# Kernel tuning notes

Measured on AMD Instinct MI355X. Metric: run time of the kernel, lower is better.

Reference implementation:

```python
import jax, jax.numpy as jnp
import numpy as np

B, T, H = 128, 256, 512


def setup_inputs() -> dict:
    key = jax.random.key(0)
    ks = jax.random.split(key, 9)
    s = 0.05  # small init scale to keep tanh/softmax well-conditioned
    return {
        "enc_output": jax.random.normal(ks[0], (B, T, H), jnp.float32),
        "h0": jax.random.normal(ks[1], (B, H), jnp.float32) * s,
        "c0": jax.random.normal(ks[2], (B, H), jnp.float32) * s,
        "W1": jax.random.normal(ks[3], (H, H), jnp.float32) * s,
        "W2": jax.random.normal(ks[4], (H, H), jnp.float32) * s,
        "V": jax.random.normal(ks[5], (H,), jnp.float32) * s,
        "Wk": jax.random.normal(ks[6], (T, 4 * H), jnp.float32) * s,  # LSTM input kernel (input = last_pointer, dim T)
        "Wr": jax.random.normal(ks[7], (H, 4 * H), jnp.float32) * s,  # LSTM recurrent kernel
        "b": jnp.zeros((4 * H,), jnp.float32),
    }


def reference(enc_output, h0, c0, W1, W2, V, Wk, Wr, b):
    Bq, Tq, Hq = enc_output.shape
    # Precompute W1 @ encoder outputs (constant across decode steps; same math)
    w1_e = jnp.einsum("bth,hd->btd", enc_output, W1)  # [B,T,H]

    def step(carry, _):
        h, c, lp = carry  # h,c: [B,H]; lp (last pointer probs): [B,T]
        z = lp @ Wk + h @ Wr + b  # [B,4H], keras gate order i,f,g,o
        i, f, g, o = jnp.split(z, 4, axis=-1)
        c_new = jax.nn.sigmoid(f) * c + jax.nn.sigmoid(i) * jnp.tanh(g)
        h_new = jax.nn.sigmoid(o) * jnp.tanh(c_new)
        # Bahdanau additive attention -> pointer distribution over T
        w2_d = h_new @ W2  # [B,H]
        score = jnp.einsum("bth,h->bt", jnp.tanh(w1_e + w2_d[:, None, :]), V)  # [B,T]
        probs = jax.nn.softmax(score, axis=1)
        return (h_new, c_new, probs), probs

    lp0 = jnp.ones((Bq, Tq), enc_output.dtype)
    _, outs = jax.lax.scan(step, (h0, c0, lp0), None, length=Tq)  # [T,B,T]
    return jnp.transpose(outs, (1, 0, 2))  # [B, T(steps), T(pointers)]
```

## Files before the change

kernel.cpp:

```cpp
#include <hip/hip_runtime.h>
#include <hip/hip_bf16.h>
#include <cstddef>

#define B_ 128
#define T_ 256
#define H_ 512
#define H4_ 2048

__device__ __forceinline__ float rcp_f(float x) { return __builtin_amdgcn_rcpf(x); }
__device__ __forceinline__ float sigf(float x) { return rcp_f(1.0f + __expf(-x)); }
__device__ __forceinline__ float tanh_f(float x) {
  float p = __expf(x + x);
  return fmaf(-2.0f, rcp_f(1.0f + p), 1.0f);
}
__device__ __forceinline__ float4 ld4(const float* p) { return *reinterpret_cast<const float4*>(p); }
__device__ __forceinline__ void st4(float* p, float4 v) { *reinterpret_cast<float4*>(p) = v; }
__device__ __forceinline__ void fma4(float4& a, float s, float4 w) {
  a.x = fmaf(s, w.x, a.x); a.y = fmaf(s, w.y, a.y);
  a.z = fmaf(s, w.z, a.z); a.w = fmaf(s, w.w, a.w);
}

__device__ __forceinline__ float ald1(const float* p) {
  return __hip_atomic_load(p, __ATOMIC_RELAXED, __HIP_MEMORY_SCOPE_AGENT);
}
__device__ __forceinline__ void ast1(float* p, float v) {
  __hip_atomic_store(p, v, __ATOMIC_RELAXED, __HIP_MEMORY_SCOPE_AGENT);
}
__device__ __forceinline__ float2 ald2(const float* p) {
  unsigned long long v = __hip_atomic_load((const unsigned long long*)p,
                                           __ATOMIC_RELAXED, __HIP_MEMORY_SCOPE_AGENT);
  union { unsigned long long u; float2 f; } c; c.u = v; return c.f;
}

union H4 { ushort4 u; _Float16 h[4]; };
union H8 { int4 v; _Float16 h[8]; };
__device__ __forceinline__ void sth4(_Float16* p, float4 v) {
  H4 c;
  c.h[0] = (_Float16)v.x; c.h[1] = (_Float16)v.y;
  c.h[2] = (_Float16)v.z; c.h[3] = (_Float16)v.w;
  *reinterpret_cast<ushort4*>(p) = c.u;
}

#define W1EH_OFF  0ull
#define WPACK_OFF 8388608ull
#define W2H_OFF   9961472ull
#define HP_OFF    10092544ull
#define HROW_OFF  10223616ull
#define EP_OFF    10289152ull
#define D2_OFF    10321920ull
#define CNT_OFF   10322432ull

__global__ __launch_bounds__(256) void w1e_kernel(const float* __restrict__ A,
                                                  const float* __restrict__ Bw,
                                                  _Float16* __restrict__ C) {
  __shared__ float As[32][68];
  __shared__ float Bs[32][68];
  const int i0 = blockIdx.x * 64;
  const int j0 = blockIdx.y * 64;
  const int tx = threadIdx.x & 15, ty = threadIdx.x >> 4;
  float4 acc0 = make_float4(0,0,0,0), acc1 = acc0, acc2 = acc0, acc3 = acc0;
  for (int k0 = 0; k0 < H_; k0 += 32) {
#pragma unroll
    for (int q = 0; q < 2; q++) {
      int idx = q * 256 + threadIdx.x;
      int ai = idx >> 3, ak = (idx & 7) << 2;
      float4 av = ld4(A + (size_t)(i0 + ai) * H_ + k0 + ak);
      As[ak][ai] = av.x; As[ak + 1][ai] = av.y; As[ak + 2][ai] = av.z; As[ak + 3][ai] = av.w;
      int bk = idx >> 4, bj = (idx & 15) << 2;
      st4(&Bs[bk][bj], ld4(Bw + (size_t)(k0 + bk) * H_ + j0 + bj));
    }
    __syncthreads();
#pragma unroll
    for (int kk = 0; kk < 32; kk++) {
      float4 a = ld4(&As[kk][ty << 2]);
      float4 bv = ld4(&Bs[kk][tx << 2]);
      fma4(acc0, a.x, bv); fma4(acc1, a.y, bv); fma4(acc2, a.z, bv); fma4(acc3, a.w, bv);
    }
    __syncthreads();
  }
  size_t base = (size_t)(i0 + (ty << 2)) * H_ + j0 + (tx << 2);
  sth4(&C[base], acc0); sth4(&C[base + H_], acc1);
  sth4(&C[base + 2 * H_], acc2); sth4(&C[base + 3 * H_], acc3);
}

__global__ __launch_bounds__(256) void pack_kernel(const float* __restrict__ Wk,
                                                   const float* __restrict__ Wr,
                                                   const float* __restrict__ W2,
                                                   float* __restrict__ Wpack,
                                                   _Float16* __restrict__ W2h,
                                                   unsigned* __restrict__ cnt) {
  const int g = blockIdx.x, tid = threadIdx.x;
#pragma unroll
  for (int it = 0; it < 24; ++it) {
    int idx = it * 256 + tid;
    int k = idx >> 3, c = idx & 7;
    int col = (c >> 1) * 512 + 2 * g + (c & 1);
    float v = (k < 256) ? Wk[(size_t)k * H4_ + col] : Wr[(size_t)(k - 256) * H4_ + col];
    Wpack[((size_t)g * 768 + k) * 8 + c] = v;
  }
#pragma unroll
  for (int it = 0; it < 4; ++it) {
    int idx = it * 65536 + g * 256 + tid;
    W2h[idx] = (_Float16)W2[idx];
  }
  if (g == 0) {
#pragma unroll
    for (int i = 0; i < 4; ++i) cnt[i * 256 + tid] = 0u;
  }
}

__device__ __forceinline__ void gridbar(unsigned* cnt, unsigned& phase, int tid, int wg) {
  asm volatile("s_waitcnt vmcnt(0)" ::: "memory");
  __syncthreads();
  if (tid == 0) {
    unsigned r1 = __hip_atomic_fetch_add(&cnt[(wg & 31) * 16], 1u,
                                         __ATOMIC_RELAXED, __HIP_MEMORY_SCOPE_AGENT);
    if (r1 == phase * 8u + 7u) {
      unsigned r2 = __hip_atomic_fetch_add(&cnt[512], 1u,
                                           __ATOMIC_RELAXED, __HIP_MEMORY_SCOPE_AGENT);
      if (r2 == phase * 32u + 31u) {
#pragma unroll
        for (int i = 0; i < 8; ++i)
          __hip_atomic_store(&cnt[768 + i * 16], phase + 1u,
                             __ATOMIC_RELAXED, __HIP_MEMORY_SCOPE_AGENT);
      }
    }
    const unsigned* rel = &cnt[768 + (wg >> 5) * 16];
    while (__hip_atomic_load(rel, __ATOMIC_RELAXED, __HIP_MEMORY_SCOPE_AGENT) <= phase)
      __builtin_amdgcn_s_sleep(2);
  }
  __syncthreads();
  ++phase;
}

__global__ __launch_bounds__(1024, 4) void decoder_persistent(
    const _Float16* __restrict__ w1eh, const float* __restrict__ Wpack,
    const _Float16* __restrict__ W2h, const float* __restrict__ Vv,
    const float* __restrict__ bias, const float* __restrict__ h0,
    const float* __restrict__ c0,
    float* __restrict__ htr,
    float* __restrict__ hrow,
    float* __restrict__ etr,
    float* __restrict__ d2,
    unsigned* __restrict__ cnt,
    float* __restrict__ out) {
  __shared__ float smem[21504];
  float* zred     = smem;
  float* zfin     = smem + 12288;
  float* c_lds    = smem + 13312;
  float* bias_lds = smem + 13568;
  float* dred     = smem + 13576;
  float* hrow_lds = smem + 13592;
  float* w2d_lds  = smem + 14104;

  const int g = blockIdx.x;
  const int tid = threadIdx.x;
  const int bl = tid & 127;
  const int ksu = __builtin_amdgcn_readfirstlane(tid >> 7);
  const int wv = tid >> 6, ln = tid & 63;
  const int sb = g >> 1;
  const int t0 = (g & 1) << 7;
  unsigned phase = 0;
  float epv[8];

  if (tid < 256) {
    int b = tid >> 1, jj = tid & 1;
    c_lds[b * 2 + jj] = c0[(size_t)b * H_ + 2 * g + jj];
    ast1(htr + 65536 + ((size_t)g * 128 + b) * 2 + jj, h0[(size_t)b * H_ + 2 * g + jj]);
    if (g == 0) ast1(d2 + 256 + tid, 0.5f);
  }
  if (tid < 8) bias_lds[tid] = bias[(tid >> 1) * 512 + 2 * g + (tid & 1)];
  if (g < 128 && tid < 256) ast1(etr + g * 256 + tid, 1.0f);
  gridbar(cnt, phase, tid, g);

  const float4 v0 = ld4(Vv + (ln << 3));
  const float4 v1 = ld4(Vv + (ln << 3) + 4);
  const _Float16* rowb = w1eh + (((size_t)sb * 256 + t0 + (wv << 3)) << 9) + (ln << 3);

  for (int s = 0; s < 256; ++s) {
    const float* hin = htr + ((s + 1) & 1) * 65536;
    float* hout = htr + (s & 1) * 65536;
    const float* dPrev = d2 + ((s + 1) & 1) * 256;
    float* dCur = d2 + (s & 1) * 256;

    H8 raws[8];
#pragma unroll
    for (int r = 0; r < 8; ++r)
      raws[r].v = *reinterpret_cast<const int4*>(rowb + ((size_t)r << 9));

    {
      float2 dd = ald2(dPrev + bl * 2);
      float rd = rcp_f(dd.x + dd.y);
      float4 accA = make_float4(0,0,0,0), accB = accA;
      float2 e0[8], e1[8];
#pragma unroll
      for (int j = 0; j < 8; ++j) {
        int k2 = ksu * 2 + j * 16;
        e0[j] = ald2(etr + k2 * 256 + bl * 2);
        e1[j] = ald2(etr + k2 * 256 + 256 + bl * 2);
      }
#pragma unroll
      for (int j = 0; j < 8; ++j) {
        int kb = ksu * 4 + j * 32;
        const float* wp = Wpack + (((size_t)g * 768 + kb) << 3);
        float4 wa0 = ld4(wp),      wb0 = ld4(wp + 4);
        float4 wa1 = ld4(wp + 8),  wb1 = ld4(wp + 12);
        float4 wa2 = ld4(wp + 16), wb2 = ld4(wp + 20);
        float4 wa3 = ld4(wp + 24), wb3 = ld4(wp + 28);
        fma4(accA, e0[j].x, wa0); fma4(accB, e0[j].x, wb0);
        fma4(accA, e0[j].y, wa1); fma4(accB, e0[j].y, wb1);
        fma4(accA, e1[j].x, wa2); fma4(accB, e1[j].x, wb2);
        fma4(accA, e1[j].y, wa3); fma4(accB, e1[j].y, wb3);
      }
      accA.x *= rd; accA.y *= rd; accA.z *= rd; accA.w *= rd;
      accB.x *= rd; accB.y *= rd; accB.z *= rd; accB.w *= rd;
#pragma unroll
      for (int half = 0; half < 2; ++half) {
        float2 p0[8], p1[8];
#pragma unroll
        for (int j = 0; j < 8; ++j) {
          int k2 = ksu * 2 + (half * 8 + j) * 16;
          p0[j] = ald2(hin + k2 * 256 + bl * 2);
          p1[j] = ald2(hin + k2 * 256 + 256 + bl * 2);
        }
#pragma unroll
        for (int j = 0; j < 8; ++j) {
          int kb = ksu * 4 + (half * 8 + j) * 32;
          const float* wp = Wpack + (((size_t)g * 768 + 256 + kb) << 3);
          float4 wa0 = ld4(wp),      wb0 = ld4(wp + 4);
          float4 wa1 = ld4(wp + 8),  wb1 = ld4(wp + 12);
          float4 wa2 = ld4(wp + 16), wb2 = ld4(wp + 20);
          float4 wa3 = ld4(wp + 24), wb3 = ld4(wp + 28);
          fma4(accA, p0[j].x, wa0); fma4(accB, p0[j].x, wb0);
          fma4(accA, p0[j].y, wa1); fma4(accB, p0[j].y, wb1);
          fma4(accA, p1[j].x, wa2); fma4(accB, p1[j].x, wb2);
          fma4(accA, p1[j].y, wa3); fma4(accB, p1[j].y, wb3);
        }
      }
      float* zr = &zred[(ksu * 128 + bl) * 12];
      st4(zr, accA); st4(zr + 4, accB);
    }
    __syncthreads();
    {
      int b = tid >> 3, cc = tid & 7;
      float zsum = bias_lds[cc];
#pragma unroll
      for (int k2 = 0; k2 < 8; ++k2) zsum += zred[(k2 * 128 + b) * 12 + cc];
      zfin[b * 8 + cc] = zsum;
    }
    __syncthreads();
    if (tid < 256) {
      int b = tid >> 1, jj = tid & 1;
      float zi = zfin[b * 8 + 0 + jj], zf = zfin[b * 8 + 2 + jj];
      float zg = zfin[b * 8 + 4 + jj], zo = zfin[b * 8 + 6 + jj];
      float cv = c_lds[b * 2 + jj];
      float cn = sigf(zf) * cv + sigf(zi) * tanh_f(zg);
      float hn = sigf(zo) * tanh_f(cn);
      c_lds[b * 2 + jj] = cn;
      ast1(hout + ((size_t)g * 128 + b) * 2 + jj, hn);
      ast1(hrow + (size_t)b * 512 + 2 * g + jj, hn);
    }
    gridbar(cnt, phase, tid, g);

    if (tid < 256) {
      float2 hv = ald2(hrow + (size_t)sb * 512 + (tid << 1));
      hrow_lds[(tid << 1)] = hv.x; hrow_lds[(tid << 1) + 1] = hv.y;
    }
    __syncthreads();
    {
      const int c8 = ln << 3;
      const _Float16* wp = W2h + ((size_t)(wv << 5) << 9) + c8;
      const float* hb = hrow_lds + (wv << 5);
      float4 accL = make_float4(0,0,0,0), accH = accL;
#pragma unroll 4
      for (int k = 0; k < 32; ++k) {
        float hk = hb[k];
        H8 w; w.v = *reinterpret_cast<const int4*>(wp + ((size_t)k << 9));
        accL.x = fmaf(hk, (float)w.h[0], accL.x);
        accL.y = fmaf(hk, (float)w.h[1], accL.y);
        accL.z = fmaf(hk, (float)w.h[2], accL.z);
        accL.w = fmaf(hk, (float)w.h[3], accL.w);
        accH.x = fmaf(hk, (float)w.h[4], accH.x);
        accH.y = fmaf(hk, (float)w.h[5], accH.y);
        accH.z = fmaf(hk, (float)w.h[6], accH.z);
        accH.w = fmaf(hk, (float)w.h[7], accH.w);
      }
      st4(&zred[(wv << 9) + c8], accL);
      st4(&zred[(wv << 9) + c8 + 4], accH);
    }
    __syncthreads();
    if (tid < 512) {
      float s16 = 0.0f;
#pragma unroll
      for (int q = 0; q < 16; ++q) s16 += zred[(q << 9) + tid];
      w2d_lds[tid] = s16;
    }
    __syncthreads();
    {
      float4 u0 = ld4(w2d_lds + (ln << 3));
      float4 u1 = ld4(w2d_lds + (ln << 3) + 4);
      float2 ddp = ald2(dPrev + sb * 2);
      float rdp = rcp_f(ddp.x + ddp.y);
      float sc[8];
#pragma unroll
      for (int r = 0; r < 8; ++r) {
        float a;
        a = tanh_f((float)raws[r].h[0] + u0.x) * v0.x;
        a = fmaf(tanh_f((float)raws[r].h[1] + u0.y), v0.y, a);
        a = fmaf(tanh_f((float)raws[r].h[2] + u0.z), v0.z, a);
        a = fmaf(tanh_f((float)raws[r].h[3] + u0.w), v0.w, a);
        a = fmaf(tanh_f((float)raws[r].h[4] + u1.x), v1.x, a);
        a = fmaf(tanh_f((float)raws[r].h[5] + u1.y), v1.y, a);
        a = fmaf(tanh_f((float)raws[r].h[6] + u1.z), v1.z, a);
        a = fmaf(tanh_f((float)raws[r].h[7] + u1.w), v1.w, a);
#pragma unroll
        for (int m = 32; m > 0; m >>= 1) a += __shfl_xor(a, m, 64);
        sc[r] = a;
      }
      if (ln == 0) {
        float dacc = 0.0f;
#pragma unroll
        for (int r = 0; r < 8; ++r) {
          int t = t0 + (wv << 3) + r;
          if (s > 0) out[(size_t)sb * 65536 + (size_t)(s - 1) * 256 + t] = epv[r] * rdp;
          float ev = __expf(sc[r]);
          epv[r] = ev;
          ast1(etr + (((t >> 1) << 7) + sb) * 2 + (t & 1), ev);
          dacc += ev;
        }
        dred[wv] = dacc;
      }
    }
    __syncthreads();
    if (tid == 0) {
      float sd = 0.0f;
#pragma unroll
      for (int k = 0; k < 16; ++k) sd += dred[k];
      ast1(dCur + sb * 2 + (g & 1), sd);
    }
    gridbar(cnt, phase, tid, g);
  }

  {
    float2 ddf = ald2(d2 + 256 + sb * 2);
    float rdf = rcp_f(ddf.x + ddf.y);
    if (ln == 0) {
#pragma unroll
      for (int r = 0; r < 8; ++r) {
        int t = t0 + (wv << 3) + r;
        out[(size_t)sb * 65536 + 255ull * 256 + t] = epv[r] * rdf;
      }
    }
  }
}

extern "C" void kernel_launch(void* const* d_in, const int* in_sizes, int n_in,
                              void* d_out, int out_size, void* d_ws, size_t ws_size,
                              hipStream_t stream) {
  const float* enc  = (const float*)d_in[0];
  const float* h0   = (const float*)d_in[1];
  const float* c0   = (const float*)d_in[2];
  const float* W1   = (const float*)d_in[3];
  const float* W2   = (const float*)d_in[4];
  const float* V    = (const float*)d_in[5];
  const float* Wk   = (const float*)d_in[6];
  const float* Wr   = (const float*)d_in[7];
  const float* bias = (const float*)d_in[8];
  float* out = (float*)d_out;
  float* ws = (float*)d_ws;

  _Float16* w1eh = (_Float16*)(ws + W1EH_OFF);
  float* Wpack   = ws + WPACK_OFF;
  _Float16* W2h  = (_Float16*)(ws + W2H_OFF);
  float* htr     = ws + HP_OFF;
  float* hrow    = ws + HROW_OFF;
  float* etr     = ws + EP_OFF;
  float* d2      = ws + D2_OFF;
  unsigned* cnt  = (unsigned*)(ws + CNT_OFF);

  pack_kernel<<<256, 256, 0, stream>>>(Wk, Wr, W2, Wpack, W2h, cnt);
  w1e_kernel<<<dim3(512, 8), 256, 0, stream>>>(enc, W1, w1eh);
  decoder_persistent<<<256, 1024, 0, stream>>>(w1eh, Wpack, W2h, V, bias, h0, c0,
                                               htr, hrow, etr, d2, cnt, out);
}
```

Before: 10.32 ms.

## Retile LSTM gate GEMV into batch×column blocks with LDS-staged inputs

The per-step LSTM gate GEMV is repartitioned. Each workgroup now owns 16 batch rows by 16 hidden columns (64 gate columns) rather than all 128 batch rows by 2 hidden columns. The e and h inputs for those 16 rows are staged into LDS once per step, with h stored as fp16, and the repacked weight slice is reused across the rows. This removes the transposed h/e copies and the duplicate hrow store, cutting global atomic loads per step. The cost is more weight traffic per workgroup, since each now reads 64 columns × 768 rows, and an fp16 rounding of h in the gate GEMV.

```diff
diff --git a/kernel.cpp b/kernel.cpp
--- a/kernel.cpp
+++ b/kernel.cpp
@@ -32,10 +32,10 @@
   union { unsigned long long u; float2 f; } c; c.u = v; return c.f;
 }
 
-union H4 { ushort4 u; _Float16 h[4]; };
-union H8 { int4 v; _Float16 h[8]; };
+union H4u { ushort4 u; _Float16 h[4]; };
+union H8u { int4 v; _Float16 h[8]; };
 __device__ __forceinline__ void sth4(_Float16* p, float4 v) {
-  H4 c;
+  H4u c;
   c.h[0] = (_Float16)v.x; c.h[1] = (_Float16)v.y;
   c.h[2] = (_Float16)v.z; c.h[3] = (_Float16)v.w;
   *reinterpret_cast<ushort4*>(p) = c.u;
@@ -44,11 +44,10 @@
 #define W1EH_OFF  0ull
 #define WPACK_OFF 8388608ull
 #define W2H_OFF   9961472ull
-#define HP_OFF    10092544ull
-#define HROW_OFF  10223616ull
-#define EP_OFF    10289152ull
-#define D2_OFF    10321920ull
-#define CNT_OFF   10322432ull
+#define HROW_OFF  10092544ull
+#define EROW_OFF  10223616ull
+#define D2_OFF    10256384ull
+#define CNT_OFF   10256896ull
 
 __global__ __launch_bounds__(256) void w1e_kernel(const float* __restrict__ A,
                                                   const float* __restrict__ Bw,
@@ -90,13 +89,15 @@
                                                    _Float16* __restrict__ W2h,
                                                    unsigned* __restrict__ cnt) {
   const int g = blockIdx.x, tid = threadIdx.x;
+  const int gblk = g >> 3, slice = g & 7;
 #pragma unroll
   for (int it = 0; it < 24; ++it) {
     int idx = it * 256 + tid;
-    int k = idx >> 3, c = idx & 7;
-    int col = (c >> 1) * 512 + 2 * g + (c & 1);
+    int kk = idx >> 6, c = idx & 63;
+    int k = slice * 96 + kk;
+    int col = (c & 3) * 512 + gblk * 16 + (c >> 2);
     float v = (k < 256) ? Wk[(size_t)k * H4_ + col] : Wr[(size_t)(k - 256) * H4_ + col];
-    Wpack[((size_t)g * 768 + k) * 8 + c] = v;
+    Wpack[((size_t)gblk * 768 + k) * 64 + c] = v;
   }
 #pragma unroll
   for (int it = 0; it < 4; ++it) {
@@ -138,132 +139,142 @@
     const _Float16* __restrict__ W2h, const float* __restrict__ Vv,
     const float* __restrict__ bias, const float* __restrict__ h0,
     const float* __restrict__ c0,
-    float* __restrict__ htr,
-    float* __restrict__ hrow,
-    float* __restrict__ etr,
+    float* __restrict__ hrowB,
+    float* __restrict__ erow,
     float* __restrict__ d2,
     unsigned* __restrict__ cnt,
     float* __restrict__ out) {
   __shared__ float smem[21504];
-  float* zred     = smem;
-  float* zfin     = smem + 12288;
-  float* c_lds    = smem + 13312;
-  float* bias_lds = smem + 13568;
-  float* dred     = smem + 13576;
-  float* hrow_lds = smem + 13592;
-  float* w2d_lds  = smem + 14104;
+  float* zred    = smem;
+  float* zfin    = smem + 8448;
+  float* stage_e = smem + 9536;
+  _Float16* stageh = (_Float16*)(smem + 13696);
+  float* c_lds   = smem + 17856;
+  float* bias64  = smem + 18112;
+  float* d_lds   = smem + 18176;
+  float* dred    = smem + 8192;
+  float* hrow_lds= smem + 8448;
+  float* w2d_lds = smem + 8960;
 
   const int g = blockIdx.x;
   const int tid = threadIdx.x;
-  const int bl = tid & 127;
-  const int ksu = __builtin_amdgcn_readfirstlane(tid >> 7);
+  const int bblk = g >> 5, cblk = g & 31;
+  const int b0 = bblk << 4;
+  const int ks = __builtin_amdgcn_readfirstlane(tid >> 7);
+  const int br = (tid >> 3) & 15;
+  const int cg = tid & 7;
   const int wv = tid >> 6, ln = tid & 63;
   const int sb = g >> 1;
   const int t0 = (g & 1) << 7;
   unsigned phase = 0;
   float epv[8];
 
+  if (tid < 64) bias64[tid] = bias[(tid & 3) * 512 + (cblk << 4) + (tid >> 2)];
   if (tid < 256) {
-    int b = tid >> 1, jj = tid & 1;
-    c_lds[b * 2 + jj] = c0[(size_t)b * H_ + 2 * g + jj];
-    ast1(htr + 65536 + ((size_t)g * 128 + b) * 2 + jj, h0[(size_t)b * H_ + 2 * g + jj]);
+    int b3 = tid >> 4, j = tid & 15;
+    int bg = b0 + b3, jg = (cblk << 4) + j;
+    c_lds[(b3 << 4) + j] = c0[(size_t)bg * H_ + jg];
+    ast1(hrowB + 65536 + (size_t)bg * 512 + jg, h0[(size_t)bg * H_ + jg]);
     if (g == 0) ast1(d2 + 256 + tid, 0.5f);
   }
-  if (tid < 8) bias_lds[tid] = bias[(tid >> 1) * 512 + 2 * g + (tid & 1)];
-  if (g < 128 && tid < 256) ast1(etr + g * 256 + tid, 1.0f);
+  if (g < 128 && tid < 256) ast1(erow + g * 256 + tid, 1.0f);
   gridbar(cnt, phase, tid, g);
 
   const float4 v0 = ld4(Vv + (ln << 3));
   const float4 v1 = ld4(Vv + (ln << 3) + 4);
   const _Float16* rowb = w1eh + (((size_t)sb * 256 + t0 + (wv << 3)) << 9) + (ln << 3);
+  const float* WpG = Wpack + (size_t)cblk * 768 * 64;
 
   for (int s = 0; s < 256; ++s) {
-    const float* hin = htr + ((s + 1) & 1) * 65536;
-    float* hout = htr + (s & 1) * 65536;
+    const float* hin = hrowB + ((s + 1) & 1) * 65536;
+    float* hout = hrowB + (s & 1) * 65536;
     const float* dPrev = d2 + ((s + 1) & 1) * 256;
     float* dCur = d2 + (s & 1) * 256;
 
-    H8 raws[8];
+    H8u raws[8];
 #pragma unroll
     for (int r = 0; r < 8; ++r)
       raws[r].v = *reinterpret_cast<const int4*>(rowb + ((size_t)r << 9));
 
     {
-      float2 dd = ald2(dPrev + bl * 2);
-      float rd = rcp_f(dd.x + dd.y);
-      float4 accA = make_float4(0,0,0,0), accB = accA;
-      float2 e0[8], e1[8];
-#pragma unroll
-      for (int j = 0; j < 8; ++j) {
-        int k2 = ksu * 2 + j * 16;
-        e0[j] = ald2(etr + k2 * 256 + bl * 2);
-        e1[j] = ald2(etr + k2 * 256 + 256 + bl * 2);
-      }
-#pragma unroll
-      for (int j = 0; j < 8; ++j) {
-        int kb = ksu * 4 + j * 32;
-        const float* wp = Wpack + (((size_t)g * 768 + kb) << 3);
-        float4 wa0 = ld4(wp),      wb0 = ld4(wp + 4);
-        float4 wa1 = ld4(wp + 8),  wb1 = ld4(wp + 12);
-        float4 wa2 = ld4(wp + 16), wb2 = ld4(wp + 20);
-        float4 wa3 = ld4(wp + 24), wb3 = ld4(wp + 28);
-        fma4(accA, e0[j].x, wa0); fma4(accB, e0[j].x, wb0);
-        fma4(accA, e0[j].y, wa1); fma4(accB, e0[j].y, wb1);
-        fma4(accA, e1[j].x, wa2); fma4(accB, e1[j].x, wb2);
-        fma4(accA, e1[j].y, wa3); fma4(accB, e1[j].y, wb3);
-      }
-      accA.x *= rd; accA.y *= rd; accA.z *= rd; accA.w *= rd;
-      accB.x *= rd; accB.y *= rd; accB.z *= rd; accB.w *= rd;
-#pragma unroll
-      for (int half = 0; half < 2; ++half) {
-        float2 p0[8], p1[8];
-#pragma unroll
-        for (int j = 0; j < 8; ++j) {
-          int k2 = ksu * 2 + (half * 8 + j) * 16;
-          p0[j] = ald2(hin + k2 * 256 + bl * 2);
-          p1[j] = ald2(hin + k2 * 256 + 256 + bl * 2);
-        }
-#pragma unroll
-        for (int j = 0; j < 8; ++j) {
-          int kb = ksu * 4 + (half * 8 + j) * 32;
-          const float* wp = Wpack + (((size_t)g * 768 + 256 + kb) << 3);
-          float4 wa0 = ld4(wp),      wb0 = ld4(wp + 4);
-          float4 wa1 = ld4(wp + 8),  wb1 = ld4(wp + 12);
-          float4 wa2 = ld4(wp + 16), wb2 = ld4(wp + 20);
-          float4 wa3 = ld4(wp + 24), wb3 = ld4(wp + 28);
-          fma4(accA, p0[j].x, wa0); fma4(accB, p0[j].x, wb0);
-          fma4(accA, p0[j].y, wa1); fma4(accB, p0[j].y, wb1);
-          fma4(accA, p1[j].x, wa2); fma4(accB, p1[j].x, wb2);
-          fma4(accA, p1[j].y, wa3); fma4(accB, p1[j].y, wb3);
-        }
-      }
-      float* zr = &zred[(ksu * 128 + bl) * 12];
-      st4(zr, accA); st4(zr + 4, accB);
-    }
-    __syncthreads();
-    {
-      int b = tid >> 3, cc = tid & 7;
-      float zsum = bias_lds[cc];
-#pragma unroll
-      for (int k2 = 0; k2 < 8; ++k2) zsum += zred[(k2 * 128 + b) * 12 + cc];
-      zfin[b * 8 + cc] = zsum;
+      int row = tid >> 6;
+      int ec = (tid & 63) << 2;
+      float2 ea = ald2(erow + (size_t)(b0 + row) * 256 + ec);
+      float2 eb = ald2(erow + (size_t)(b0 + row) * 256 + ec + 2);
+      st4(&stage_e[row * 260 + ec], make_float4(ea.x, ea.y, eb.x, eb.y));
+      int hc = (tid & 63) << 3;
+      const float* hp = hin + (size_t)(b0 + row) * 512 + hc;
+      float2 h0v = ald2(hp), h1v = ald2(hp + 2), h2v = ald2(hp + 4), h3v = ald2(hp + 6);
+      sth4(&stageh[row * 520 + hc], make_float4(h0v.x, h0v.y, h1v.x, h1v.y));
+      sth4(&stageh[row * 520 + hc + 4], make_float4(h2v.x, h2v.y, h3v.x, h3v.y));
+      if (tid < 16) {
+        float2 dd = ald2(dPrev + (b0 + tid) * 2);
+        d_lds[tid] = dd.x + dd.y;
+      }
+    }
+    __syncthreads();
+    {
+      float4 aE0 = make_float4(0,0,0,0), aE1 = aE0, aH0 = aE0, aH1 = aE0;
+#pragma unroll
+      for (int kk = 0; kk < 32; kk += 4) {
+        float4 ev = ld4(&stage_e[br * 260 + (ks << 5) + kk]);
+        const float* wp = WpG + (size_t)((ks << 5) + kk) * 64 + (cg << 3);
+        float4 w00 = ld4(wp),       w01 = ld4(wp + 4);
+        float4 w10 = ld4(wp + 64),  w11 = ld4(wp + 68);
+        float4 w20 = ld4(wp + 128), w21 = ld4(wp + 132);
+        float4 w30 = ld4(wp + 192), w31 = ld4(wp + 196);
+        fma4(aE0, ev.x, w00); fma4(aE1, ev.x, w01);
+        fma4(aE0, ev.y, w10); fma4(aE1, ev.y, w11);
+        fma4(aE0, ev.z, w20); fma4(aE1, ev.z, w21);
+        fma4(aE0, ev.w, w30); fma4(aE1, ev.w, w31);
+      }
+#pragma unroll 4
+      for (int kk = 0; kk < 64; kk += 4) {
+        H4u hv; hv.u = *reinterpret_cast<const ushort4*>(&stageh[br * 520 + (ks << 6) + kk]);
+        const float* wp = WpG + (size_t)(256 + (ks << 6) + kk) * 64 + (cg << 3);
+        float4 w00 = ld4(wp),       w01 = ld4(wp + 4);
+        float4 w10 = ld4(wp + 64),  w11 = ld4(wp + 68);
+        float4 w20 = ld4(wp + 128), w21 = ld4(wp + 132);
+        float4 w30 = ld4(wp + 192), w31 = ld4(wp + 196);
+        fma4(aH0, (float)hv.h[0], w00); fma4(aH1, (float)hv.h[0], w01);
+        fma4(aH0, (float)hv.h[1], w10); fma4(aH1, (float)hv.h[1], w11);
+        fma4(aH0, (float)hv.h[2], w20); fma4(aH1, (float)hv.h[2], w21);
+        fma4(aH0, (float)hv.h[3], w30); fma4(aH1, (float)hv.h[3], w31);
+      }
+      float rd = rcp_f(d_lds[br]);
+      float4 z0, z1;
+      z0.x = fmaf(aE0.x, rd, aH0.x); z0.y = fmaf(aE0.y, rd, aH0.y);
+      z0.z = fmaf(aE0.z, rd, aH0.z); z0.w = fmaf(aE0.w, rd, aH0.w);
+      z1.x = fmaf(aE1.x, rd, aH1.x); z1.y = fmaf(aE1.y, rd, aH1.y);
+      z1.z = fmaf(aE1.z, rd, aH1.z); z1.w = fmaf(aE1.w, rd, aH1.w);
+      float* zr = &zred[((ks << 4) + br) * 66 + (cg << 3)];
+      st4(zr, z0); st4(zr + 4, z1);
+    }
+    __syncthreads();
+    {
+      int b2 = tid >> 6, c2 = tid & 63;
+      float zs = bias64[c2];
+#pragma unroll
+      for (int k2 = 0; k2 < 8; ++k2) zs += zred[((k2 << 4) + b2) * 66 + c2];
+      zfin[b2 * 68 + c2] = zs;
     }
     __syncthreads();
     if (tid < 256) {
-      int b = tid >> 1, jj = tid & 1;
-      float zi = zfin[b * 8 + 0 + jj], zf = zfin[b * 8 + 2 + jj];
-      float zg = zfin[b * 8 + 4 + jj], zo = zfin[b * 8 + 6 + jj];
-      float cv = c_lds[b * 2 + jj];
+      int b3 = tid >> 4, j = tid & 15;
+      float zi = zfin[b3 * 68 + (j << 2) + 0];
+      float zf = zfin[b3 * 68 + (j << 2) + 1];
+      float zg = zfin[b3 * 68 + (j << 2) + 2];
+      float zo = zfin[b3 * 68 + (j << 2) + 3];
+      float cv = c_lds[(b3 << 4) + j];
       float cn = sigf(zf) * cv + sigf(zi) * tanh_f(zg);
       float hn = sigf(zo) * tanh_f(cn);
-      c_lds[b * 2 + jj] = cn;
-      ast1(hout + ((size_t)g * 128 + b) * 2 + jj, hn);
-      ast1(hrow + (size_t)b * 512 + 2 * g + jj, hn);
+      c_lds[(b3 << 4) + j] = cn;
+      ast1(hout + (size_t)(b0 + b3) * 512 + (cblk << 4) + j, hn);
     }
     gridbar(cnt, phase, tid, g);
 
     if (tid < 256) {
-      float2 hv = ald2(hrow + (size_t)sb * 512 + (tid << 1));
+      float2 hv = ald2(hout + (size_t)sb * 512 + (tid << 1));
       hrow_lds[(tid << 1)] = hv.x; hrow_lds[(tid << 1) + 1] = hv.y;
     }
     __syncthreads();
@@ -275,7 +286,7 @@
 #pragma unroll 4
       for (int k = 0; k < 32; ++k) {
         float hk = hb[k];
-        H8 w; w.v = *reinterpret_cast<const int4*>(wp + ((size_t)k << 9));
+        H8u w; w.v = *reinterpret_cast<const int4*>(wp + ((size_t)k << 9));
         accL.x = fmaf(hk, (float)w.h[0], accL.x);
         accL.y = fmaf(hk, (float)w.h[1], accL.y);
         accL.z = fmaf(hk, (float)w.h[2], accL.z);
@@ -325,7 +336,7 @@
           if (s > 0) out[(size_t)sb * 65536 + (size_t)(s - 1) * 256 + t] = epv[r] * rdp;
           float ev = __expf(sc[r]);
           epv[r] = ev;
-          ast1(etr + (((t >> 1) << 7) + sb) * 2 + (t & 1), ev);
+          ast1(erow + (size_t)sb * 256 + t, ev);
           dacc += ev;
         }
         dred[wv] = dacc;
@@ -372,14 +383,13 @@
   _Float16* w1eh = (_Float16*)(ws + W1EH_OFF);
   float* Wpack   = ws + WPACK_OFF;
   _Float16* W2h  = (_Float16*)(ws + W2H_OFF);
-  float* htr     = ws + HP_OFF;
-  float* hrow    = ws + HROW_OFF;
-  float* etr     = ws + EP_OFF;
+  float* hrowB   = ws + HROW_OFF;
+  float* erow    = ws + EROW_OFF;
   float* d2      = ws + D2_OFF;
   unsigned* cnt  = (unsigned*)(ws + CNT_OFF);
 
   pack_kernel<<<256, 256, 0, stream>>>(Wk, Wr, W2, Wpack, W2h, cnt);
   w1e_kernel<<<dim3(512, 8), 256, 0, stream>>>(enc, W1, w1eh);
   decoder_persistent<<<256, 1024, 0, stream>>>(w1eh, Wpack, W2h, V, bias, h0, c0,
-                                               htr, hrow, etr, d2, cnt, out);
-}
+                                               hrowB, erow, d2, cnt, out);
+}
```

Result: slower. 31.82 ms (+208.2%).
